# Kernel tuning notes

Hardware: AMD Instinct MI355X
Metric: run time of the kernel (lower is better)

The kernel has to match this reference:

```python
import jax, jax.numpy as jnp
import numpy as np

K = 3          # kernel_size
PAD = K // 2   # same-size unfold padding
R = 4          # num_rules


def _unfold(x, k=K, pad=PAD):
    """F.unfold equivalent: [B,C,H,W] -> [B,C,k*k,H*W], row-major (row,col) patch order."""
    B, C, H, W = x.shape
    xp = jnp.pad(x, ((0, 0), (0, 0), (pad, pad), (pad, pad)))
    patches = jnp.stack([xp[:, :, r:r + H, c:c + W] for r in range(k) for c in range(k)], axis=2)
    return patches.reshape(B, C, k * k, H * W)


def _offsets(k=K):
    """(dx, dy) offsets matching unfold patch order; shape [1,1,S,1]."""
    dy = jnp.array([float(r - k // 2) for r in range(k) for c in range(k)], jnp.float32).reshape(1, 1, k * k, 1)
    dx = jnp.array([float(c - k // 2) for r in range(k) for c in range(k)], jnp.float32).reshape(1, 1, k * k, 1)
    return dx, dy


def setup_inputs() -> dict:
    key = jax.random.key(0)
    ks = jax.random.split(key, 8)
    B, C, H, W, Cout = 8, 64, 128, 128, 64
    sc = 0.1
    return {
        "x": jax.random.normal(ks[0], (B, C, H, W), jnp.float32),
        "gate_w": jax.random.normal(ks[1], (R, C), jnp.float32) * sc,       # gate_conv 1x1
        "gate_b": jnp.zeros((R,), jnp.float32),
        "value_w": jax.random.normal(ks[2], (C, C), jnp.float32) * sc,      # value_conv 1x1, no bias
        "geom_w": jax.random.normal(ks[3], (3 * R, C), jnp.float32) * sc,   # geometry_conv 1x1
        "geom_b": jax.random.normal(ks[4], (3 * R,), jnp.float32) * sc,
        "pw_w": jax.random.normal(ks[5], (Cout, R * C), jnp.float32) * sc,  # pointwise 1x1
        "pw_b": jnp.zeros((Cout,), jnp.float32),
    }


def reference(x, gate_w, gate_b, value_w, geom_w, geom_b, pw_w, pw_b):
    B, C, H, W = x.shape
    S, L = K * K, H * W
    dx, dy = _offsets()

    # fuzzy rule memberships [B,R,H,W] (softmax over rules)
    gate = jnp.einsum('rc,bchw->brhw', gate_w, x) + gate_b[None, :, None, None]
    mu = jax.nn.softmax(gate, axis=1)

    # local hyperbolic geometry: per-point theta / base / hyperbolicity fields
    geom = jnp.einsum('gc,bchw->bghw', geom_w, x) + geom_b[None, :, None, None]
    theta_map, raw_base, raw_hyper = jnp.split(geom, 3, axis=1)
    base_map = jax.nn.softplus(raw_base) + 1e-4
    hyper_map = jax.nn.softplus(raw_hyper)

    theta_c = theta_map.reshape(B, R, 1, L)
    base_c = base_map.reshape(B, R, 1, L)
    hyper_c = hyper_map.reshape(B, R, 1, L)
    theta_n = _unfold(theta_map)  # [B,R,S,L]
    base_n = _unfold(base_map)
    hyper_n = _unfold(hyper_map)

    # symmetrize direction across center/neighbor via doubled-angle averaging
    c2 = jnp.cos(2.0 * theta_c) + jnp.cos(2.0 * theta_n)
    s2 = jnp.sin(2.0 * theta_c) + jnp.sin(2.0 * theta_n)
    nrm = jnp.maximum(jnp.sqrt(c2 ** 2 + s2 ** 2), 1e-6)
    theta_pair = 0.5 * jnp.arctan2(s2 / nrm, c2 / nrm)
    u_x = jnp.cos(theta_pair)
    u_y = jnp.sin(theta_pair)

    base_p = 0.5 * (base_c + base_n)
    hyper_p = 0.5 * (hyper_c + hyper_n)
    sigma_u = base_p * jnp.exp(hyper_p)
    sigma_s = base_p * jnp.exp(-hyper_p)

    proj_u = u_x * dx + u_y * dy
    proj_s = -u_y * dx + u_x * dy
    kern = jnp.exp(-proj_u ** 2 / sigma_u ** 2 - proj_s ** 2 / sigma_s ** 2)  # [B,R,S,L]

    # raw compatibilities = geometry kernel * fuzzy neighbor membership; normalize over S
    mu_n = _unfold(mu)                                  # [B,R,S,L]
    compat = kern * mu_n
    w = compat / (jnp.sum(compat, axis=2, keepdims=True) + 1e-6)

    # value projection + per-rule neighbor aggregation
    v = jnp.einsum('dc,bchw->bdhw', value_w, x)
    v_un = _unfold(v)                                   # [B,C,S,L]
    agg = jnp.einsum('brsl,bcsl->brcl', w, v_un).reshape(B, R * C, H, W)

    # 1x1 pointwise mix of rules x channels
    out = jnp.einsum('om,bmhw->bohw', pw_w, agg) + pw_b[None, :, None, None]
    return out
```

## Files before the change

### kernel.cpp

```cpp
#include <hip/hip_runtime.h>

namespace {
constexpr int Bx = 8, Cc = 64, Hh = 128, Ww = 128, Co = 64;
constexpr int Ll = Hh * Ww;
constexpr int NPIX = Bx * Ll;
constexpr int TP = 64;
}

using short8 = __attribute__((ext_vector_type(8))) short;
using f32x4  = __attribute__((ext_vector_type(4))) float;

__device__ __forceinline__ unsigned short f32_to_bf16(float f) {
    union { float f; unsigned u; } un; un.f = f;
    unsigned r = un.u + 0x7FFFu + ((un.u >> 16) & 1u);
    return (unsigned short)(r >> 16);
}
__device__ __forceinline__ unsigned cvt_pk_bf16(float lo, float hi) {
    unsigned u;
    asm("v_cvt_pk_bf16_f32 %0, %1, %2" : "=v"(u) : "v"(lo), "v"(hi));
    return u;
}
__device__ __forceinline__ float bflo(unsigned u) {
    union { unsigned x; float f; } c; c.x = u << 16; return c.f;
}
__device__ __forceinline__ float bfhi(unsigned u) {
    union { unsigned x; float f; } c; c.x = u & 0xFFFF0000u; return c.f;
}

__global__ __launch_bounds__(256) void k0_pack_weights(
    const float* __restrict__ gate_w,
    const float* __restrict__ geom_w,
    const float* __restrict__ value_w,
    const float* __restrict__ pw_w,
    float* __restrict__ wt16,
    unsigned short* __restrict__ vwb16,
    unsigned short* __restrict__ pwb16)
{
    for (int idx = threadIdx.x; idx < Cc * 16; idx += 256) {
        const int c = idx >> 4, j = idx & 15;
        wt16[idx] = (j < 4) ? gate_w[j * Cc + c] : geom_w[(j - 4) * Cc + c];
    }
    for (int flat = threadIdx.x; flat < 4096; flat += 256) {
        const int t    = flat >> 10;
        const int ks   = (flat >> 9) & 1;
        const int lane = (flat >> 3) & 63;
        const int jj   = flat & 7;
        const int j = t * 16 + (lane & 15);
        const int c = ks * 32 + ((lane >> 4) & 3) * 8 + jj;
        vwb16[flat] = f32_to_bf16(value_w[j * Cc + c]);
    }
    for (int idx = threadIdx.x; idx < Co * 256; idx += 256) {
        const int o = idx >> 8, m = idx & 255;
        const int r = m >> 6, c = m & 63;
        pwb16[o * 256 + c * 4 + r] = f32_to_bf16(pw_w[idx]);
    }
}

__device__ __forceinline__ float softplusf(float v) {
    return v > 20.f ? v : log1pf(__expf(v));
}

__global__ __launch_bounds__(256) void k1_project(
    const float* __restrict__ x,
    const unsigned short* __restrict__ vwb16,
    const float* __restrict__ wt16,
    const float* __restrict__ gate_b,
    const float* __restrict__ geom_b,
    float* __restrict__ v,
    float* __restrict__ mu,
    float* __restrict__ cs2, float* __restrict__ sn2,
    float* __restrict__ bse, float* __restrict__ hyp)
{
    __shared__ unsigned short xb16[64][72];
    __shared__ float part[4][64][17];

    const int tid  = threadIdx.x;
    const int px   = tid & 63;
    const int ch   = tid >> 6;
    const int lane = tid & 63;
    const int pix0 = blockIdx.x * 64;
    const int b    = pix0 >> 14;
    const int l0   = pix0 & (Ll - 1);

    float acc[16];
#pragma unroll
    for (int j = 0; j < 16; ++j) acc[j] = 0.f;

    const float* xb = x + (size_t)b * Cc * Ll + (l0 + px);
#pragma unroll
    for (int j0 = 0; j0 < 16; j0 += 8) {
        float xv[8];
#pragma unroll
        for (int j = 0; j < 8; ++j) xv[j] = xb[(size_t)(ch * 16 + j0 + j) * Ll];
        uint4 ph;
        unsigned* hp = (unsigned*)&ph;
#pragma unroll
        for (int j = 0; j < 4; ++j)
            hp[j] = cvt_pk_bf16(xv[2 * j], xv[2 * j + 1]);
        *(uint4*)&xb16[px][ch * 16 + j0] = ph;
#pragma unroll
        for (int j = 0; j < 8; ++j) {
            const float* wr = wt16 + (ch * 16 + j0 + j) * 16;
#pragma unroll
            for (int jj = 0; jj < 16; ++jj) acc[jj] = fmaf(wr[jj], xv[j], acc[jj]);
        }
    }
#pragma unroll
    for (int jj = 0; jj < 16; ++jj) part[ch][px][jj] = acc[jj];

    short8 af[8];
#pragma unroll
    for (int i = 0; i < 8; ++i)
        af[i] = *(const short8*)(vwb16 + ((size_t)(i * 64 + lane)) * 8);

    __syncthreads();

    {
        const int g = ch;
        const int l = l0 + px;
        const size_t fb = (size_t)b * 4 * Ll + l;
        float o[4];
#pragma unroll
        for (int q = 0; q < 4; ++q)
            o[q] = part[0][px][4 * g + q] + part[1][px][4 * g + q]
                 + part[2][px][4 * g + q] + part[3][px][4 * g + q];
        if (g == 0) {
            float e[4], gm = -1e30f;
#pragma unroll
            for (int q = 0; q < 4; ++q) { e[q] = o[q] + gate_b[q]; gm = fmaxf(gm, e[q]); }
            float gs = 0.f;
#pragma unroll
            for (int q = 0; q < 4; ++q) { e[q] = __expf(e[q] - gm); gs += e[q]; }
            const float gi = __fdividef(1.f, gs);
#pragma unroll
            for (int q = 0; q < 4; ++q) mu[fb + (size_t)q * Ll] = e[q] * gi;
        } else if (g == 1) {
#pragma unroll
            for (int q = 0; q < 4; ++q) {
                float sv, cv;
                __sincosf(2.f * (o[q] + geom_b[q]), &sv, &cv);
                cs2[fb + (size_t)q * Ll] = cv;
                sn2[fb + (size_t)q * Ll] = sv;
            }
        } else if (g == 2) {
#pragma unroll
            for (int q = 0; q < 4; ++q)
                bse[fb + (size_t)q * Ll] = softplusf(o[q] + geom_b[4 + q]) + 1e-4f;
        } else {
#pragma unroll
            for (int q = 0; q < 4; ++q)
                hyp[fb + (size_t)q * Ll] = softplusf(o[q] + geom_b[8 + q]);
        }
    }

    const int px16 = lane & 15;
    const int g2   = lane >> 4;
    {
        const int row = ch * 16 + px16;
        const short8 bh0 = *(const short8*)&xb16[row][g2 * 8];
        const short8 bh1 = *(const short8*)&xb16[row][32 + g2 * 8];

        f32x4 d0, d1, d2, d3;
#define PROJ_TILE(dst, t)                                              \
        {                                                              \
            f32x4 a_ = {0.f, 0.f, 0.f, 0.f};                           \
            a_ = __builtin_amdgcn_mfma_f32_16x16x32_bf16(af[2*(t)],   bh0, a_, 0, 0, 0); \
            a_ = __builtin_amdgcn_mfma_f32_16x16x32_bf16(af[2*(t)+1], bh1, a_, 0, 0, 0); \
            dst = a_;                                                  \
        }
        PROJ_TILE(d0, 0) PROJ_TILE(d1, 1) PROJ_TILE(d2, 2) PROJ_TILE(d3, 3)
#undef PROJ_TILE

        const int l = l0 + ch * 16 + px16;
        float* vrow = v + ((size_t)b * Ll + l) * 64 + g2 * 4;
        *(f32x4*)(vrow)      = d0;
        *(f32x4*)(vrow + 16) = d1;
        *(f32x4*)(vrow + 32) = d2;
        *(f32x4*)(vrow + 48) = d3;
    }
}

__global__ __launch_bounds__(256, 4) void k23_fused(
    const float* __restrict__ mu,
    const float* __restrict__ cs2, const float* __restrict__ sn2,
    const float* __restrict__ bse, const float* __restrict__ hyp,
    const float* __restrict__ v,
    const unsigned short* __restrict__ pwb16,
    const float* __restrict__ pw_b,
    float* __restrict__ out)
{
    __shared__ unsigned wqpk[4][64][6];
    __shared__ unsigned short agg[TP][264];

    const int tid = threadIdx.x;
    const int cpx = (int)(gridDim.x >> 3);
    const int bid = (int)((blockIdx.x & 7) * cpx + (blockIdx.x >> 3));
    const int pix0 = bid * TP;
    const int b = pix0 >> 14;
    const int l0 = pix0 & (Ll - 1);

    {
        const int px = tid & 63;
        const int r  = tid >> 6;
        const int l  = l0 + px;
        const int hr = l >> 7;
        const int wc = l & (Ww - 1);
        const size_t fb = ((size_t)b * 4 + r) * Ll;

        const float cc = cs2[fb + l], sc = sn2[fb + l];
        const float bc = bse[fb + l], yc = hyp[fb + l];
        const float mc = mu[fb + l];

        float cmp[9];
        float sum = 0.f;
#pragma unroll
        for (int s = 0; s < 9; ++s) {
            const int dy = s / 3 - 1, dx = s % 3 - 1;
            float cv;
            if (dx == 0 && dy == 0) {
                cv = mc;
            } else {
                const int hh = hr + dy, ww = wc + dx;
                const int hcl = min(max(hh, 0), Hh - 1);
                const int wcl = min(max(ww, 0), Ww - 1);
                const bool inb = ((unsigned)hh < (unsigned)Hh) &
                                 ((unsigned)ww < (unsigned)Ww);
                const size_t ni = fb + hcl * Ww + wcl;
                const float cn = cs2[ni], sn = sn2[ni];
                const float bn = bse[ni], yn = hyp[ni];
                const float mun = inb ? mu[ni] : 0.f;
                const float c2 = cc + cn, s2 = sc + sn;
                const float h = sqrtf(fmaxf(c2 * c2 + s2 * s2, 1e-24f));
                const float rh = __fdividef(0.5f, h);
                float pu2, ps2;
                if (dx != 0 && dy != 0) {
                    const float t = 2.f * (float)(dx * dy) * (s2 * rh);
                    pu2 = 1.f + t; ps2 = 1.f - t;
                } else if (dx != 0) {
                    pu2 = 0.5f + c2 * rh; ps2 = 0.5f - c2 * rh;
                } else {
                    pu2 = 0.5f - c2 * rh; ps2 = 0.5f + c2 * rh;
                }
                const float bp = 0.5f * (bc + bn);
                const float hp = 0.5f * (yc + yn);
                const float E = __expf(hp);
                const float iu = __fdividef(1.f, bp * E);
                const float is = E * E * iu;
                const float q = pu2 * (iu * iu) + ps2 * (is * is);
                cv = __expf(-q) * mun;
            }
            cmp[s] = cv;
            sum += cv;
        }
        const float inv = __fdividef(1.f, sum + 1e-6f);
        unsigned* wrow = &wqpk[r][px][0];
#pragma unroll
        for (int k = 0; k < 4; ++k)
            wrow[k] = cvt_pk_bf16(cmp[2 * k] * inv, cmp[2 * k + 1] * inv);
        wrow[4] = cvt_pk_bf16(cmp[8] * inv, 0.f);
    }
    __syncthreads();

    const int w = tid >> 6, c = tid & 63;
    {
        const int hr0  = l0 >> 7;
        const int rows[3] = { max(hr0 - 1, 0) * Ww, hr0 * Ww, min(hr0 + 1, Hh - 1) * Ww };
        const int colbase = (l0 & (Ww - 1)) + w * 16;
        const float* vb = v + ((size_t)b * Ll) * 64 + c;

        float vv[3][18];
#pragma unroll
        for (int ry = 0; ry < 3; ++ry)
#pragma unroll
            for (int cx = 0; cx < 18; ++cx) {
                const int col = min(max(colbase + cx - 1, 0), Ww - 1);
                vv[ry][cx] = vb[(size_t)(rows[ry] + col) * 64];
            }

#pragma unroll
        for (int p = 0; p < 16; ++p) {
            float av[4];
#pragma unroll
            for (int r = 0; r < 4; ++r) {
                const unsigned* wrow = &wqpk[r][w * 16 + p][0];
                const unsigned u0 = wrow[0], u1 = wrow[1], u2 = wrow[2],
                               u3 = wrow[3], u4 = wrow[4];
                float a;
                a = bflo(u0) * vv[0][p];
                a = fmaf(bfhi(u0), vv[0][p + 1], a);
                a = fmaf(bflo(u1), vv[0][p + 2], a);
                a = fmaf(bfhi(u1), vv[1][p],     a);
                a = fmaf(bflo(u2), vv[1][p + 1], a);
                a = fmaf(bfhi(u2), vv[1][p + 2], a);
                a = fmaf(bflo(u3), vv[2][p],     a);
                a = fmaf(bfhi(u3), vv[2][p + 1], a);
                a = fmaf(bflo(u4), vv[2][p + 2], a);
                av[r] = a;
            }
            uint2 u;
            u.x = cvt_pk_bf16(av[0], av[1]);
            u.y = cvt_pk_bf16(av[2], av[3]);
            *((uint2*)(&agg[w * 16 + p][0]) + c) = u;
        }
    }

    const int ar    = tid & 15;
    const int chunk = (tid >> 4) & 3;
    const int o0    = w * 16;
    const unsigned short* aPtr = pwb16 + (o0 + ar) * 256 + chunk * 8;
    short8 af[8];
#pragma unroll
    for (int kt = 0; kt < 8; ++kt) af[kt] = *(const short8*)(aPtr + kt * 32);

    __syncthreads();

    f32x4 d0, d1, d2, d3;
#pragma unroll
    for (int q = 0; q < 4; ++q) {
        const float bv = pw_b[o0 + chunk * 4 + q];
        d0[q] = bv; d1[q] = bv; d2[q] = bv; d3[q] = bv;
    }
    const unsigned short* b0 = &agg[ 0 + ar][chunk * 8];
    const unsigned short* b1 = &agg[16 + ar][chunk * 8];
    const unsigned short* b2 = &agg[32 + ar][chunk * 8];
    const unsigned short* b3 = &agg[48 + ar][chunk * 8];
#pragma unroll
    for (int kt = 0; kt < 8; ++kt) {
        d0 = __builtin_amdgcn_mfma_f32_16x16x32_bf16(af[kt], *(const short8*)(b0 + kt * 32), d0, 0, 0, 0);
        d1 = __builtin_amdgcn_mfma_f32_16x16x32_bf16(af[kt], *(const short8*)(b1 + kt * 32), d1, 0, 0, 0);
        d2 = __builtin_amdgcn_mfma_f32_16x16x32_bf16(af[kt], *(const short8*)(b2 + kt * 32), d2, 0, 0, 0);
        d3 = __builtin_amdgcn_mfma_f32_16x16x32_bf16(af[kt], *(const short8*)(b3 + kt * 32), d3, 0, 0, 0);
    }

#pragma unroll
    for (int q = 0; q < 4; ++q) {
        const int o = o0 + chunk * 4 + q;
        float* ob = out + ((size_t)b * Co + o) * Ll + l0 + ar;
        ob[0]  = d0[q];
        ob[16] = d1[q];
        ob[32] = d2[q];
        ob[48] = d3[q];
    }
}

extern "C" void kernel_launch(void* const* d_in, const int* in_sizes, int n_in,
                              void* d_out, int out_size, void* d_ws, size_t ws_size,
                              hipStream_t stream)
{
    const float* x       = (const float*)d_in[0];
    const float* gate_w  = (const float*)d_in[1];
    const float* gate_b  = (const float*)d_in[2];
    const float* value_w = (const float*)d_in[3];
    const float* geom_w  = (const float*)d_in[4];
    const float* geom_b  = (const float*)d_in[5];
    const float* pw_w    = (const float*)d_in[6];
    const float* pw_b    = (const float*)d_in[7];
    float* out = (float*)d_out;

    float* ws  = (float*)d_ws;
    float* v    = ws;
    float* mu   = v    + (size_t)Bx * Ll * 64;
    float* cs2  = mu   + (size_t)Bx * 4 * Ll;
    float* sn2  = cs2  + (size_t)Bx * 4 * Ll;
    float* bse  = sn2  + (size_t)Bx * 4 * Ll;
    float* hyp  = bse  + (size_t)Bx * 4 * Ll;
    float* wt16 = hyp  + (size_t)Bx * 4 * Ll;
    unsigned short* vwb16 = (unsigned short*)(wt16 + 1024);
    unsigned short* pwb16 = vwb16 + 4096;

    k0_pack_weights<<<1, 256, 0, stream>>>(gate_w, geom_w, value_w, pw_w,
                                           wt16, vwb16, pwb16);
    k1_project<<<NPIX / 64, 256, 0, stream>>>(x, vwb16, wt16, gate_b, geom_b,
                                              v, mu, cs2, sn2, bse, hyp);
    k23_fused<<<NPIX / TP, 256, 0, stream>>>(mu, cs2, sn2, bse, hyp,
                                             v, pwb16, pw_b, out);
}
```

Before: 75.26 us.

## Store value projection as bf16 and interleave per-pixel geometry fields

The value projection intermediate is now stored as packed bf16 instead of fp32, halving its write and read traffic between the two kernels. The five per-rule field planes (mu, cos, sin, base, hyper) are interleaved into a 32-float per-pixel record, so each neighbor lookup is two 16-byte vector loads instead of five scattered scalar loads. The shared-memory weight table is re-laid out so each pixel's 20 packed weights load as uint4 vectors. In exchange, v now carries bf16 rounding error, and the padded field layout writes more bytes than the five planes did.

```diff
diff --git a/kernel.cpp b/kernel.cpp
--- a/kernel.cpp
+++ b/kernel.cpp
@@ -66,10 +66,8 @@
     const float* __restrict__ wt16,
     const float* __restrict__ gate_b,
     const float* __restrict__ geom_b,
-    float* __restrict__ v,
-    float* __restrict__ mu,
-    float* __restrict__ cs2, float* __restrict__ sn2,
-    float* __restrict__ bse, float* __restrict__ hyp)
+    unsigned* __restrict__ v_pk,
+    float* __restrict__ fld)
 {
     __shared__ unsigned short xb16[64][72];
     __shared__ float part[4][64][17];
@@ -118,7 +116,7 @@
     {
         const int g = ch;
         const int l = l0 + px;
-        const size_t fb = (size_t)b * 4 * Ll + l;
+        float* fo = fld + ((size_t)b * Ll + l) * 32;
         float o[4];
 #pragma unroll
         for (int q = 0; q < 4; ++q)
@@ -133,23 +131,29 @@
             for (int q = 0; q < 4; ++q) { e[q] = __expf(e[q] - gm); gs += e[q]; }
             const float gi = __fdividef(1.f, gs);
 #pragma unroll
-            for (int q = 0; q < 4; ++q) mu[fb + (size_t)q * Ll] = e[q] * gi;
+            for (int q = 0; q < 4; ++q) {
+                float2 wv; wv.x = e[q] * gi; wv.y = 0.f;
+                *(float2*)(fo + q * 8 + 6) = wv;
+            }
         } else if (g == 1) {
 #pragma unroll
             for (int q = 0; q < 4; ++q) {
-                float sv, cv;
-                __sincosf(2.f * (o[q] + geom_b[q]), &sv, &cv);
-                cs2[fb + (size_t)q * Ll] = cv;
-                sn2[fb + (size_t)q * Ll] = sv;
+                float2 wv;
+                __sincosf(2.f * (o[q] + geom_b[q]), &wv.y, &wv.x);
+                *(float2*)(fo + q * 8 + 0) = wv;
             }
         } else if (g == 2) {
 #pragma unroll
-            for (int q = 0; q < 4; ++q)
-                bse[fb + (size_t)q * Ll] = softplusf(o[q] + geom_b[4 + q]) + 1e-4f;
+            for (int q = 0; q < 4; ++q) {
+                float2 wv; wv.x = softplusf(o[q] + geom_b[4 + q]) + 1e-4f; wv.y = 0.f;
+                *(float2*)(fo + q * 8 + 2) = wv;
+            }
         } else {
 #pragma unroll
-            for (int q = 0; q < 4; ++q)
-                hyp[fb + (size_t)q * Ll] = softplusf(o[q] + geom_b[8 + q]);
+            for (int q = 0; q < 4; ++q) {
+                float2 wv; wv.x = softplusf(o[q] + geom_b[8 + q]); wv.y = 0.f;
+                *(float2*)(fo + q * 8 + 4) = wv;
+            }
         }
     }
 
@@ -172,24 +176,27 @@
 #undef PROJ_TILE
 
         const int l = l0 + ch * 16 + px16;
-        float* vrow = v + ((size_t)b * Ll + l) * 64 + g2 * 4;
-        *(f32x4*)(vrow)      = d0;
-        *(f32x4*)(vrow + 16) = d1;
-        *(f32x4*)(vrow + 32) = d2;
-        *(f32x4*)(vrow + 48) = d3;
+        unsigned* vp = v_pk + ((size_t)b * Ll + l) * 32 + g2 * 2;
+        uint2 u;
+        u.x = cvt_pk_bf16(d0[0], d0[1]); u.y = cvt_pk_bf16(d0[2], d0[3]);
+        *(uint2*)(vp)      = u;
+        u.x = cvt_pk_bf16(d1[0], d1[1]); u.y = cvt_pk_bf16(d1[2], d1[3]);
+        *(uint2*)(vp + 8)  = u;
+        u.x = cvt_pk_bf16(d2[0], d2[1]); u.y = cvt_pk_bf16(d2[2], d2[3]);
+        *(uint2*)(vp + 16) = u;
+        u.x = cvt_pk_bf16(d3[0], d3[1]); u.y = cvt_pk_bf16(d3[2], d3[3]);
+        *(uint2*)(vp + 24) = u;
     }
 }
 
 __global__ __launch_bounds__(256, 4) void k23_fused(
-    const float* __restrict__ mu,
-    const float* __restrict__ cs2, const float* __restrict__ sn2,
-    const float* __restrict__ bse, const float* __restrict__ hyp,
-    const float* __restrict__ v,
+    const float* __restrict__ fld,
+    const unsigned* __restrict__ v_pk,
     const unsigned short* __restrict__ pwb16,
     const float* __restrict__ pw_b,
     float* __restrict__ out)
 {
-    __shared__ unsigned wqpk[4][64][6];
+    __shared__ unsigned wqpk[64 * 24];
     __shared__ unsigned short agg[TP][264];
 
     const int tid = threadIdx.x;
@@ -205,11 +212,12 @@
         const int l  = l0 + px;
         const int hr = l >> 7;
         const int wc = l & (Ww - 1);
-        const size_t fb = ((size_t)b * 4 + r) * Ll;
-
-        const float cc = cs2[fb + l], sc = sn2[fb + l];
-        const float bc = bse[fb + l], yc = hyp[fb + l];
-        const float mc = mu[fb + l];
+        const float* fbase = fld + (size_t)b * Ll * 32 + r * 8;
+
+        const float* fc = fbase + (size_t)l * 32;
+        const f32x4 c0 = *(const f32x4*)fc;
+        const f32x4 c1 = *(const f32x4*)(fc + 4);
+        const float cc = c0[0], sc = c0[1], bc = c0[2], yc = c1[0], mc = c1[2];
 
         float cmp[9];
         float sum = 0.f;
@@ -225,10 +233,11 @@
                 const int wcl = min(max(ww, 0), Ww - 1);
                 const bool inb = ((unsigned)hh < (unsigned)Hh) &
                                  ((unsigned)ww < (unsigned)Ww);
-                const size_t ni = fb + hcl * Ww + wcl;
-                const float cn = cs2[ni], sn = sn2[ni];
-                const float bn = bse[ni], yn = hyp[ni];
-                const float mun = inb ? mu[ni] : 0.f;
+                const float* fn = fbase + (size_t)(hcl * Ww + wcl) * 32;
+                const f32x4 n0 = *(const f32x4*)fn;
+                const f32x4 n1 = *(const f32x4*)(fn + 4);
+                const float cn = n0[0], sn = n0[1], bn = n0[2], yn = n1[0];
+                const float mun = inb ? n1[2] : 0.f;
                 const float c2 = cc + cn, s2 = sc + sn;
                 const float h = sqrtf(fmaxf(c2 * c2 + s2 * s2, 1e-24f));
                 const float rh = __fdividef(0.5f, h);
@@ -253,7 +262,7 @@
             sum += cv;
         }
         const float inv = __fdividef(1.f, sum + 1e-6f);
-        unsigned* wrow = &wqpk[r][px][0];
+        unsigned* wrow = &wqpk[px * 24 + r * 5];
 #pragma unroll
         for (int k = 0; k < 4; ++k)
             wrow[k] = cvt_pk_bf16(cmp[2 * k] * inv, cmp[2 * k + 1] * inv);
@@ -266,7 +275,8 @@
         const int hr0  = l0 >> 7;
         const int rows[3] = { max(hr0 - 1, 0) * Ww, hr0 * Ww, min(hr0 + 1, Hh - 1) * Ww };
         const int colbase = (l0 & (Ww - 1)) + w * 16;
-        const float* vb = v + ((size_t)b * Ll) * 64 + c;
+        const unsigned* vb = v_pk + (size_t)b * Ll * 32 + (c >> 1);
+        const int hi = c & 1;
 
         float vv[3][18];
 #pragma unroll
@@ -274,17 +284,25 @@
 #pragma unroll
             for (int cx = 0; cx < 18; ++cx) {
                 const int col = min(max(colbase + cx - 1, 0), Ww - 1);
-                vv[ry][cx] = vb[(size_t)(rows[ry] + col) * 64];
+                const unsigned u = vb[(size_t)(rows[ry] + col) * 32];
+                vv[ry][cx] = hi ? bfhi(u) : bflo(u);
             }
 
 #pragma unroll
         for (int p = 0; p < 16; ++p) {
+            const unsigned* wrow = &wqpk[(w * 16 + p) * 24];
+            unsigned wu[20];
+            *(uint4*)(wu)      = *(const uint4*)(wrow);
+            *(uint4*)(wu + 4)  = *(const uint4*)(wrow + 4);
+            *(uint4*)(wu + 8)  = *(const uint4*)(wrow + 8);
+            *(uint4*)(wu + 12) = *(const uint4*)(wrow + 12);
+            *(uint4*)(wu + 16) = *(const uint4*)(wrow + 16);
             float av[4];
 #pragma unroll
             for (int r = 0; r < 4; ++r) {
-                const unsigned* wrow = &wqpk[r][w * 16 + p][0];
-                const unsigned u0 = wrow[0], u1 = wrow[1], u2 = wrow[2],
-                               u3 = wrow[3], u4 = wrow[4];
+                const unsigned u0 = wu[5 * r], u1 = wu[5 * r + 1],
+                               u2 = wu[5 * r + 2], u3 = wu[5 * r + 3],
+                               u4 = wu[5 * r + 4];
                 float a;
                 a = bflo(u0) * vv[0][p];
                 a = fmaf(bfhi(u0), vv[0][p + 1], a);
@@ -357,21 +375,15 @@
     const float* pw_b    = (const float*)d_in[7];
     float* out = (float*)d_out;
 
-    float* ws  = (float*)d_ws;
-    float* v    = ws;
-    float* mu   = v    + (size_t)Bx * Ll * 64;
-    float* cs2  = mu   + (size_t)Bx * 4 * Ll;
-    float* sn2  = cs2  + (size_t)Bx * 4 * Ll;
-    float* bse  = sn2  + (size_t)Bx * 4 * Ll;
-    float* hyp  = bse  + (size_t)Bx * 4 * Ll;
-    float* wt16 = hyp  + (size_t)Bx * 4 * Ll;
+    unsigned* v_pk = (unsigned*)d_ws;
+    float* fld  = (float*)(v_pk + (size_t)Bx * Ll * 32);
+    float* wt16 = fld + (size_t)Bx * Ll * 32;
     unsigned short* vwb16 = (unsigned short*)(wt16 + 1024);
     unsigned short* pwb16 = vwb16 + 4096;
 
     k0_pack_weights<<<1, 256, 0, stream>>>(gate_w, geom_w, value_w, pw_w,
                                            wt16, vwb16, pwb16);
     k1_project<<<NPIX / 64, 256, 0, stream>>>(x, vwb16, wt16, gate_b, geom_b,
-                                              v, mu, cs2, sn2, bse, hyp);
-    k23_fused<<<NPIX / TP, 256, 0, stream>>>(mu, cs2, sn2, bse, hyp,
-                                             v, pwb16, pw_b, out);
-}
+                                              v_pk, fld);
+    k23_fused<<<NPIX / TP, 256, 0, stream>>>(fld, v_pk, pwb16, pw_b, out);
+}
```

Result: slower. 93.76 us (+24.6%).

## Halve fused kernel pixel tile and raise occupancy; parallelize weight packing

Applied to the files above, without the earlier changes.

Cuts the fused aggregation/pointwise kernel tile from 64 to 32 pixels per block, which shrinks the per-thread value register window (3x18 to 3x10), the LDS footprint and the MFMA accumulators, and raises the launch-bounds occupancy target from 4 to 8 blocks. Only half the threads now compute the neighbour weights, and the packed weight layout is reordered to match. The weight-packing kernel is spread over 8 blocks instead of 1. Trade-off: more redundant halo loads of v per pixel and idle threads during the weight phase.

```diff
diff --git a/kernel.cpp b/kernel.cpp
--- a/kernel.cpp
+++ b/kernel.cpp
@@ -4,7 +4,7 @@
 constexpr int Bx = 8, Cc = 64, Hh = 128, Ww = 128, Co = 64;
 constexpr int Ll = Hh * Ww;
 constexpr int NPIX = Bx * Ll;
-constexpr int TP = 64;
+constexpr int TP = 32;
 }
 
 using short8 = __attribute__((ext_vector_type(8))) short;
@@ -36,11 +36,12 @@
     unsigned short* __restrict__ vwb16,
     unsigned short* __restrict__ pwb16)
 {
-    for (int idx = threadIdx.x; idx < Cc * 16; idx += 256) {
+    const int tid0 = blockIdx.x * 256 + threadIdx.x;
+    for (int idx = tid0; idx < Cc * 16; idx += 2048) {
         const int c = idx >> 4, j = idx & 15;
         wt16[idx] = (j < 4) ? gate_w[j * Cc + c] : geom_w[(j - 4) * Cc + c];
     }
-    for (int flat = threadIdx.x; flat < 4096; flat += 256) {
+    for (int flat = tid0; flat < 4096; flat += 2048) {
         const int t    = flat >> 10;
         const int ks   = (flat >> 9) & 1;
         const int lane = (flat >> 3) & 63;
@@ -49,7 +50,7 @@
         const int c = ks * 32 + ((lane >> 4) & 3) * 8 + jj;
         vwb16[flat] = f32_to_bf16(value_w[j * Cc + c]);
     }
-    for (int idx = threadIdx.x; idx < Co * 256; idx += 256) {
+    for (int idx = tid0; idx < Co * 256; idx += 2048) {
         const int o = idx >> 8, m = idx & 255;
         const int r = m >> 6, c = m & 63;
         pwb16[o * 256 + c * 4 + r] = f32_to_bf16(pw_w[idx]);
@@ -180,7 +181,7 @@
     }
 }
 
-__global__ __launch_bounds__(256, 4) void k23_fused(
+__global__ __launch_bounds__(256, 8) void k23_fused(
     const float* __restrict__ mu,
     const float* __restrict__ cs2, const float* __restrict__ sn2,
     const float* __restrict__ bse, const float* __restrict__ hyp,
@@ -189,7 +190,7 @@
     const float* __restrict__ pw_b,
     float* __restrict__ out)
 {
-    __shared__ unsigned wqpk[4][64][6];
+    __shared__ unsigned wqpk[4][TP][6];
     __shared__ unsigned short agg[TP][264];
 
     const int tid = threadIdx.x;
@@ -199,9 +200,9 @@
     const int b = pix0 >> 14;
     const int l0 = pix0 & (Ll - 1);
 
-    {
-        const int px = tid & 63;
-        const int r  = tid >> 6;
+    if (tid < 128) {
+        const int px = tid & 31;
+        const int r  = (tid >> 5) & 3;
         const int l  = l0 + px;
         const int hr = l >> 7;
         const int wc = l & (Ww - 1);
@@ -254,9 +255,10 @@
         }
         const float inv = __fdividef(1.f, sum + 1e-6f);
         unsigned* wrow = &wqpk[r][px][0];
-#pragma unroll
-        for (int k = 0; k < 4; ++k)
-            wrow[k] = cvt_pk_bf16(cmp[2 * k] * inv, cmp[2 * k + 1] * inv);
+        wrow[0] = cvt_pk_bf16(cmp[0] * inv, cmp[1] * inv);
+        wrow[1] = cvt_pk_bf16(cmp[3] * inv, cmp[4] * inv);
+        wrow[2] = cvt_pk_bf16(cmp[6] * inv, cmp[7] * inv);
+        wrow[3] = cvt_pk_bf16(cmp[2] * inv, cmp[5] * inv);
         wrow[4] = cvt_pk_bf16(cmp[8] * inv, 0.f);
     }
     __syncthreads();
@@ -265,42 +267,42 @@
     {
         const int hr0  = l0 >> 7;
         const int rows[3] = { max(hr0 - 1, 0) * Ww, hr0 * Ww, min(hr0 + 1, Hh - 1) * Ww };
-        const int colbase = (l0 & (Ww - 1)) + w * 16;
+        const int colbase = (l0 & (Ww - 1)) + w * 8;
         const float* vb = v + ((size_t)b * Ll) * 64 + c;
 
-        float vv[3][18];
+        float vv[3][10];
 #pragma unroll
         for (int ry = 0; ry < 3; ++ry)
 #pragma unroll
-            for (int cx = 0; cx < 18; ++cx) {
+            for (int cx = 0; cx < 10; ++cx) {
                 const int col = min(max(colbase + cx - 1, 0), Ww - 1);
                 vv[ry][cx] = vb[(size_t)(rows[ry] + col) * 64];
             }
 
 #pragma unroll
-        for (int p = 0; p < 16; ++p) {
+        for (int p = 0; p < 8; ++p) {
             float av[4];
 #pragma unroll
             for (int r = 0; r < 4; ++r) {
-                const unsigned* wrow = &wqpk[r][w * 16 + p][0];
+                const unsigned* wrow = &wqpk[r][w * 8 + p][0];
                 const unsigned u0 = wrow[0], u1 = wrow[1], u2 = wrow[2],
                                u3 = wrow[3], u4 = wrow[4];
                 float a;
                 a = bflo(u0) * vv[0][p];
                 a = fmaf(bfhi(u0), vv[0][p + 1], a);
-                a = fmaf(bflo(u1), vv[0][p + 2], a);
-                a = fmaf(bfhi(u1), vv[1][p],     a);
-                a = fmaf(bflo(u2), vv[1][p + 1], a);
-                a = fmaf(bfhi(u2), vv[1][p + 2], a);
-                a = fmaf(bflo(u3), vv[2][p],     a);
-                a = fmaf(bfhi(u3), vv[2][p + 1], a);
+                a = fmaf(bflo(u3), vv[0][p + 2], a);
+                a = fmaf(bflo(u1), vv[1][p],     a);
+                a = fmaf(bfhi(u1), vv[1][p + 1], a);
+                a = fmaf(bfhi(u3), vv[1][p + 2], a);
+                a = fmaf(bflo(u2), vv[2][p],     a);
+                a = fmaf(bfhi(u2), vv[2][p + 1], a);
                 a = fmaf(bflo(u4), vv[2][p + 2], a);
                 av[r] = a;
             }
             uint2 u;
             u.x = cvt_pk_bf16(av[0], av[1]);
             u.y = cvt_pk_bf16(av[2], av[3]);
-            *((uint2*)(&agg[w * 16 + p][0]) + c) = u;
+            *((uint2*)(&agg[w * 8 + p][0]) + c) = u;
         }
     }
 
@@ -314,22 +316,18 @@
 
     __syncthreads();
 
-    f32x4 d0, d1, d2, d3;
+    f32x4 d0, d1;
 #pragma unroll
     for (int q = 0; q < 4; ++q) {
         const float bv = pw_b[o0 + chunk * 4 + q];
-        d0[q] = bv; d1[q] = bv; d2[q] = bv; d3[q] = bv;
+        d0[q] = bv; d1[q] = bv;
     }
     const unsigned short* b0 = &agg[ 0 + ar][chunk * 8];
     const unsigned short* b1 = &agg[16 + ar][chunk * 8];
-    const unsigned short* b2 = &agg[32 + ar][chunk * 8];
-    const unsigned short* b3 = &agg[48 + ar][chunk * 8];
 #pragma unroll
     for (int kt = 0; kt < 8; ++kt) {
         d0 = __builtin_amdgcn_mfma_f32_16x16x32_bf16(af[kt], *(const short8*)(b0 + kt * 32), d0, 0, 0, 0);
         d1 = __builtin_amdgcn_mfma_f32_16x16x32_bf16(af[kt], *(const short8*)(b1 + kt * 32), d1, 0, 0, 0);
-        d2 = __builtin_amdgcn_mfma_f32_16x16x32_bf16(af[kt], *(const short8*)(b2 + kt * 32), d2, 0, 0, 0);
-        d3 = __builtin_amdgcn_mfma_f32_16x16x32_bf16(af[kt], *(const short8*)(b3 + kt * 32), d3, 0, 0, 0);
     }
 
 #pragma unroll
@@ -338,8 +336,6 @@
         float* ob = out + ((size_t)b * Co + o) * Ll + l0 + ar;
         ob[0]  = d0[q];
         ob[16] = d1[q];
-        ob[32] = d2[q];
-        ob[48] = d3[q];
     }
 }
 
@@ -368,7 +364,7 @@
     unsigned short* vwb16 = (unsigned short*)(wt16 + 1024);
     unsigned short* pwb16 = vwb16 + 4096;
 
-    k0_pack_weights<<<1, 256, 0, stream>>>(gate_w, geom_w, value_w, pw_w,
+    k0_pack_weights<<<8, 256, 0, stream>>>(gate_w, geom_w, value_w, pw_w,
                                            wt16, vwb16, pwb16);
     k1_project<<<NPIX / 64, 256, 0, stream>>>(x, vwb16, wt16, gate_b, geom_b,
                                               v, mu, cs2, sn2, bse, hyp);
```

Result: faster. 70.55 us (median of 4 runs) (-6.3%).
